# Kernel tuning notes

Measured on AMD Instinct MI355X. Metric: run time of the kernel, lower is better.

The kernel has to match this reference:

```python
import jax, jax.numpy as jnp
import numpy as np

T, L, N, DR = 8, 8, 500, 32
D = 2 * DR          # dr2 = 64
K = 12              # neighbors per region
S = 2               # number_sp attention layers


def setup_inputs() -> dict:
    key = jax.random.key(0)
    ks = jax.random.split(key, 14)
    inp = {}
    inp["all_data_static"] = jax.random.normal(ks[0], (T, L, N, D), jnp.float32)
    inp["thre_nc"] = jax.random.uniform(ks[1], (T, L, N, 1), jnp.float32)
    inp["all_data_dynamic_now"] = jax.random.uniform(ks[2], (L, N, D), jnp.float32)
    inp["neigh_poi"] = jax.random.randint(ks[3], (N, K), 0, N)
    inp["neigh_road"] = jax.random.randint(ks[4], (N, K), 0, N)
    inp["neigh_record"] = jax.random.randint(ks[5], (N, K), 0, N)
    inp["w1"] = jax.random.normal(ks[6], (2 * D, D), jnp.float32) * 0.05
    inp["wq_all"] = jax.random.normal(ks[7], (2, 3, S, D, D), jnp.float32) * 0.05
    inp["wk_all"] = jax.random.normal(ks[8], (2, 3, S, D, D), jnp.float32) * 0.05
    inp["wd_all"] = jax.random.normal(ks[9], (2, 3, S, D, D), jnp.float32) * 0.05
    inp["wmix_all"] = jax.random.normal(ks[10], (2, 3, D), jnp.float32) * 0.1
    inp["conv_w"] = jax.random.normal(ks[11], (4, 2 * D + 1), jnp.float32) * 0.05
    inp["conv_b"] = jnp.zeros((4,), jnp.float32)
    inp["fin_w"] = jax.random.normal(ks[12], (N, N), jnp.float32) * 0.02
    inp["fin_b"] = jnp.ones((N,), jnp.float32)
    return inp


def _attention(data, neigh, wq, wk, wd):
    # data: (T,L,N,D), neigh: (N,K)
    dn = data[:, :, neigh, :]                                   # (T,L,N,K,D) gather
    q = jnp.einsum('tlnd,de->tlne', data, wq)                   # (T,L,N,D)
    k = jnp.einsum('tlnkd,de->tlnke', dn, wk)                   # (T,L,N,K,D)
    a = jax.nn.softmax(jnp.einsum('tlne,tlnke->tlnk', q, k), -1)
    out = q + jnp.einsum('tlnk,tlnke->tlne', a, k)              # residual on q
    return jax.nn.sigmoid(jnp.einsum('tlnd,de->tlne', out, wd))


def _multiattention(data, neighs, wq, wk, wd, wmix):
    outs = []
    for g in range(3):  # poi, road, record
        x = data
        for s in range(wq.shape[1]):
            x = _attention(x, neighs[g], wq[g, s], wk[g, s], wd[g, s])
        outs.append(x)
    return jax.nn.sigmoid(outs[0] * wmix[0] + outs[1] * wmix[1] + outs[2] * wmix[2])


def reference(all_data_static, thre_nc, all_data_dynamic_now,
              neigh_poi, neigh_road, neigh_record,
              w1, wq_all, wk_all, wd_all, wmix_all,
              conv_w, conv_b, fin_w, fin_b):
    # --- Evolution: gated recurrence over time steps 1..T-1 ---
    def evo_step(now, xs):
        st, th = xs  # (L,N,D), (L,N,1)
        new = jax.nn.sigmoid(jnp.concatenate([now, st], -1) @ w1 * th
                             + now * (1.0 - th))
        return new, (new, new - now)
    now_final, (dyn_rest, diffs) = jax.lax.scan(
        evo_step, all_data_dynamic_now, (all_data_static[1:], thre_nc[1:]))
    all_dyn = jnp.concatenate([all_data_dynamic_now[None], dyn_rest], 0)  # (T,L,N,D)

    neighs = (neigh_poi, neigh_road, neigh_record)
    dyn = _multiattention(all_dyn, neighs, wq_all[0], wk_all[0], wd_all[0], wmix_all[0])
    sta = _multiattention(all_data_static, neighs, wq_all[1], wk_all[1], wd_all[1], wmix_all[1])
    x = jnp.concatenate([dyn, sta], -1)                          # (T,L,N,2D)

    # --- ConvLSTM, kernel (1,1), hidden_dim=1 -> pointwise gated recurrence ---
    h0 = jnp.zeros((x.shape[0], x.shape[2], 1), x.dtype)         # (T,N,1)
    def cell(carry, xt):  # xt: (T,N,2D)
        h, c = carry
        gates = jnp.concatenate([xt, h], -1) @ conv_w.T + conv_b  # (T,N,4)
        i = jax.nn.sigmoid(gates[..., 0:1])
        f = jax.nn.sigmoid(gates[..., 1:2])
        o = jax.nn.sigmoid(gates[..., 2:3])
        g = jnp.tanh(gates[..., 3:4])
        c2 = f * c + i * g
        h2 = o * jnp.tanh(c2)
        return (h2, c2), None
    (h_last, _), _ = jax.lax.scan(cell, (h0, h0), jnp.swapaxes(x, 0, 1))

    out = jax.nn.sigmoid(h_last[..., 0] @ fin_w.T + fin_b)       # (T,N)
    return out, now_final, diffs
```

## Files before the change

kernel.cpp:

```cpp
#include <hip/hip_runtime.h>
#include <math.h>

namespace {
constexpr int kT = 8, kL = 8, kN = 500, kD = 64, kK = 12;
constexpr int kLN  = kL * kN;
constexpr int kTLN = kT * kL * kN;
constexpr int kBUF = kTLN * kD;
constexpr int XS = 68;
constexpr int EVR = 16;
}

__device__ __forceinline__ float sigf(float v) { return 1.f / (1.f + __expf(-v)); }

__device__ __forceinline__ float tanh_fast(float v) {
    float e = __expf(-2.f * fabsf(v));
    float t = (1.f - e) / (1.f + e);
    return copysignf(t, v);
}

__device__ __forceinline__ float row_allreduce16(float v) {
    v += __int_as_float(__builtin_amdgcn_update_dpp(
            0, __float_as_int(v), 0xB1, 0xf, 0xf, true));
    v += __int_as_float(__builtin_amdgcn_update_dpp(
            0, __float_as_int(v), 0x4E, 0xf, 0xf, true));
    v += __int_as_float(__builtin_amdgcn_update_dpp(
            0, __float_as_int(v), 0x124, 0xf, 0xf, true));
    v += __int_as_float(__builtin_amdgcn_update_dpp(
            0, __float_as_int(v), 0x128, 0xf, 0xf, true));
    return v;
}

__device__ __forceinline__ void stage_x(const float* __restrict__ src, float* lds,
                                        int row0) {
    int r  = threadIdx.x >> 4;
    int c4 = (threadIdx.x & 15) << 2;
#pragma unroll
    for (int i = 0; i < 4; ++i) {
        int rr  = r + 16 * i;
        float4 v = *reinterpret_cast<const float4*>(src + (size_t)(row0 + rr) * 64 + c4);
        *reinterpret_cast<float4*>(lds + rr * XS + c4) = v;
    }
}

template <int K>
__device__ __forceinline__ void stage_w(const float* __restrict__ w, float* lds) {
    const float4* s = reinterpret_cast<const float4*>(w);
    float4* d = reinterpret_cast<float4*>(lds);
#pragma unroll
    for (int i = 0; i < K / 16; ++i)
        d[threadIdx.x + 256 * i] = s[threadIdx.x + 256 * i];
}

__device__ __forceinline__ void gemm_core_gw(const float* ldsx,
                                             const float* __restrict__ gw,
                                             int rblk, int cblk, float4 acc[4]) {
#pragma unroll 4
    for (int k = 0; k < 64; k += 4) {
        float4 xv[4], wv[4];
#pragma unroll
        for (int i = 0; i < 4; ++i)
            xv[i] = *reinterpret_cast<const float4*>(ldsx + (4 * rblk + i) * XS + k);
#pragma unroll
        for (int d = 0; d < 4; ++d)
            wv[d] = *reinterpret_cast<const float4*>(gw + (k + d) * 64 + 4 * cblk);
#pragma unroll
        for (int i = 0; i < 4; ++i) {
            float xs[4] = {xv[i].x, xv[i].y, xv[i].z, xv[i].w};
#pragma unroll
            for (int d = 0; d < 4; ++d) {
                acc[i].x = fmaf(xs[d], wv[d].x, acc[i].x);
                acc[i].y = fmaf(xs[d], wv[d].y, acc[i].y);
                acc[i].z = fmaf(xs[d], wv[d].z, acc[i].z);
                acc[i].w = fmaf(xs[d], wv[d].w, acc[i].w);
            }
        }
    }
}

__device__ __forceinline__ void gemm_core2_bal(const float* ldsx, const float* ldswa,
                                               const float* __restrict__ gwb,
                                               int rblk, int cblk,
                                               float4 acca[4], float4 accb[4]) {
#pragma unroll 4
    for (int k = 0; k < 64; k += 4) {
        float4 xv[4], wa[4], wb[4];
#pragma unroll
        for (int i = 0; i < 4; ++i)
            xv[i] = *reinterpret_cast<const float4*>(ldsx + (4 * rblk + i) * XS + k);
#pragma unroll
        for (int d = 0; d < 4; ++d) {
            wa[d] = *reinterpret_cast<const float4*>(ldswa + (k + d) * 64 + 4 * cblk);
            wb[d] = *reinterpret_cast<const float4*>(gwb + (k + d) * 64 + 4 * cblk);
        }
#pragma unroll
        for (int i = 0; i < 4; ++i) {
            float xs[4] = {xv[i].x, xv[i].y, xv[i].z, xv[i].w};
#pragma unroll
            for (int d = 0; d < 4; ++d) {
                acca[i].x = fmaf(xs[d], wa[d].x, acca[i].x);
                acca[i].y = fmaf(xs[d], wa[d].y, acca[i].y);
                acca[i].z = fmaf(xs[d], wa[d].z, acca[i].z);
                acca[i].w = fmaf(xs[d], wa[d].w, acca[i].w);
                accb[i].x = fmaf(xs[d], wb[d].x, accb[i].x);
                accb[i].y = fmaf(xs[d], wb[d].y, accb[i].y);
                accb[i].z = fmaf(xs[d], wb[d].z, accb[i].z);
                accb[i].w = fmaf(xs[d], wb[d].w, accb[i].w);
            }
        }
    }
}

__device__ __forceinline__ void gemm_qk_body(const float* __restrict__ X,
                                             const float* __restrict__ wq,
                                             const float* __restrict__ wk,
                                             float* __restrict__ b1c,
                                             float* __restrict__ b2c,
                                             int row0, float* ldsx, float* ldswq) {
    stage_x(X, ldsx, row0);
    stage_w<64>(wq, ldswq);
    __syncthreads();
    int rblk = threadIdx.x >> 4, cblk = threadIdx.x & 15;
    float4 aq[4] = {}, ak[4] = {};
    gemm_core2_bal(ldsx, ldswq, wk, rblk, cblk, aq, ak);
#pragma unroll
    for (int i = 0; i < 4; ++i) {
        size_t row = row0 + 4 * rblk + i;
        *reinterpret_cast<float4*>(b1c + row * 64 + 4 * cblk) = aq[i];
        *reinterpret_cast<float4*>(b2c + row * 64 + 4 * cblk) = ak[i];
    }
}

__global__ void __launch_bounds__(256) evo_statqk_kernel(
        const float* __restrict__ stat, const float* __restrict__ thre,
        const float* __restrict__ dyn0, float* __restrict__ all_dyn,
        float* __restrict__ diff, float* __restrict__ now_final,
        const float* __restrict__ w1, const float* __restrict__ wq_all,
        const float* __restrict__ wk_all, float* __restrict__ b1,
        float* __restrict__ b2) {
    __shared__ float lds[2 * EVR * XS + 128 * 64];
    if (blockIdx.x < kLN / EVR) {
        float* ldsn = lds;
        float* ldss = lds + EVR * XS;
        float* ldsw = lds + 2 * EVR * XS;
        int row0 = blockIdx.x * EVR;
        int r  = threadIdx.x >> 4;
        int c4 = (threadIdx.x & 15) << 2;
        *reinterpret_cast<float4*>(ldsn + r * XS + c4) =
            *reinterpret_cast<const float4*>(dyn0 + (size_t)(row0 + r) * 64 + c4);
        stage_w<128>(w1, ldsw);
        __syncthreads();
        {
            float4 x0 = *reinterpret_cast<const float4*>(ldsn + r * XS + c4);
            *reinterpret_cast<float4*>(all_dyn + (size_t)(row0 + r) * 64 + c4) = x0;
        }
#pragma unroll 1
        for (int t = 1; t < kT; ++t) {
            *reinterpret_cast<float4*>(ldss + r * XS + c4) =
                *reinterpret_cast<const float4*>(stat + (size_t)t * kLN * kD
                                                 + (size_t)(row0 + r) * 64 + c4);
            __syncthreads();
            float4 acc = {0.f, 0.f, 0.f, 0.f};
#pragma unroll 4
            for (int k = 0; k < 64; k += 4) {
                float4 xv = *reinterpret_cast<const float4*>(ldsn + r * XS + k);
                float xs[4] = {xv.x, xv.y, xv.z, xv.w};
#pragma unroll
                for (int d = 0; d < 4; ++d) {
                    float4 wv = *reinterpret_cast<const float4*>(ldsw + (k + d) * 64 + c4);
                    acc.x = fmaf(xs[d], wv.x, acc.x);
                    acc.y = fmaf(xs[d], wv.y, acc.y);
                    acc.z = fmaf(xs[d], wv.z, acc.z);
                    acc.w = fmaf(xs[d], wv.w, acc.w);
                }
            }
#pragma unroll 4
            for (int k = 0; k < 64; k += 4) {
                float4 xv = *reinterpret_cast<const float4*>(ldss + r * XS + k);
                float xs[4] = {xv.x, xv.y, xv.z, xv.w};
#pragma unroll
                for (int d = 0; d < 4; ++d) {
                    float4 wv = *reinterpret_cast<const float4*>(ldsw + (64 + k + d) * 64 + c4);
                    acc.x = fmaf(xs[d], wv.x, acc.x);
                    acc.y = fmaf(xs[d], wv.y, acc.y);
                    acc.z = fmaf(xs[d], wv.z, acc.z);
                    acc.w = fmaf(xs[d], wv.w, acc.w);
                }
            }
            int row = row0 + r;
            float tt = thre[t * kLN + row];
            float4 xn = *reinterpret_cast<const float4*>(ldsn + r * XS + c4);
            float4 nv;
            nv.x = sigf(acc.x * tt + xn.x * (1.f - tt));
            nv.y = sigf(acc.y * tt + xn.y * (1.f - tt));
            nv.z = sigf(acc.z * tt + xn.z * (1.f - tt));
            nv.w = sigf(acc.w * tt + xn.w * (1.f - tt));
            float4 df;
            df.x = nv.x - xn.x; df.y = nv.y - xn.y;
            df.z = nv.z - xn.z; df.w = nv.w - xn.w;
            *reinterpret_cast<float4*>(all_dyn + ((size_t)t * kLN + row) * 64 + c4) = nv;
            *reinterpret_cast<float4*>(diff + ((size_t)(t - 1) * kLN + row) * 64 + c4) = df;
            if (t == kT - 1)
                *reinterpret_cast<float4*>(now_final + (size_t)row * 64 + c4) = nv;
            __syncthreads();
            *reinterpret_cast<float4*>(ldsn + r * XS + c4) = nv;
        }
    } else {
        int b = blockIdx.x - kLN / EVR;
        int c = 3 + b / 500;
        int tile = b - (c - 3) * 500;
        float* b1c = b1 + (size_t)c * kBUF;
        float* b2c = b2 + (size_t)c * kBUF;
        size_t woff = (size_t)(c * 2) * kD * kD;
        gemm_qk_body(stat, wq_all + woff, wk_all + woff, b1c, b2c,
                     tile * 64, lds, lds + 64 * XS);
    }
}

__global__ void __launch_bounds__(256) gemm_qk(const float* __restrict__ Xdyn,
                                               const float* __restrict__ Xstat,
                                               const float* __restrict__ wq_all,
                                               const float* __restrict__ wk_all,
                                               float* __restrict__ b1,
                                               float* __restrict__ b2, int step) {
    __shared__ float ldsx[64 * XS];
    __shared__ float ldswq[64 * 64];
    int c = blockIdx.y;
    int m = c / 3;
    float* b1c = b1 + (size_t)c * kBUF;
    float* b2c = b2 + (size_t)c * kBUF;
    const float* X = step ? b1c : (m == 0 ? Xdyn : Xstat);
    size_t woff = (size_t)(c * 2 + step) * kD * kD;
    gemm_qk_body(X, wq_all + woff, wk_all + woff, b1c, b2c,
                 blockIdx.x * 64, ldsx, ldswq);
}

__global__ void __launch_bounds__(256) scorewd_kernel(float* __restrict__ b1,
                                                      const float* __restrict__ b2,
                                                      const int* __restrict__ npoi,
                                                      const int* __restrict__ nroad,
                                                      const int* __restrict__ nrec,
                                                      const float* __restrict__ wd_all,
                                                      int step) {
    __shared__ float ldsx[64 * XS];
    int p   = blockIdx.y * gridDim.x + blockIdx.x;
    int xcd = p & 7;
    int gid = xcd * 375 + (p >> 3);
    int c    = gid / 500;
    int tile = gid - c * 500;
    int g = c % 3;
    float* b1c = b1 + (size_t)c * kBUF;
    const float* b2c = b2 + (size_t)c * kBUF;
    const int* neigh = (g == 0) ? npoi : (g == 1) ? nroad : nrec;
    const float* gw = wd_all + (size_t)(c * 2 + step) * kD * kD;

    int lane = threadIdx.x & 63;
    int wv   = threadIdx.x >> 6;
    int sub  = lane >> 4;
    int gq   = lane & 15;
    int row0 = tile * 64;
#pragma unroll 1
    for (int pp = 0; pp < 4; ++pp) {
        int lr  = pp * 16 + wv * 4 + sub;
        int row = row0 + lr;
        int n   = row % kN;
        int slab = row - n;
        float4 q = *(reinterpret_cast<const float4*>(b1c) + (size_t)row * 16 + gq);
        const int4* nbp = reinterpret_cast<const int4*>(neigh + n * kK);
        int4 nb0 = nbp[0], nb1 = nbp[1], nb2 = nbp[2];
        int nb[12] = {nb0.x, nb0.y, nb0.z, nb0.w, nb1.x, nb1.y, nb1.z, nb1.w,
                      nb2.x, nb2.y, nb2.z, nb2.w};
        float4 kv[12];
        float sc[12];
#pragma unroll
        for (int j = 0; j < 12; ++j) {
            kv[j] = *(reinterpret_cast<const float4*>(b2c) + (size_t)(slab + nb[j]) * 16 + gq);
            sc[j] = q.x * kv[j].x + q.y * kv[j].y + q.z * kv[j].z + q.w * kv[j].w;
        }
#pragma unroll
        for (int j = 0; j < 12; ++j) sc[j] = row_allreduce16(sc[j]);
        float mx = sc[0];
#pragma unroll
        for (int j = 1; j < 12; ++j) mx = fmaxf(mx, sc[j]);
        float ssum = 0.f;
#pragma unroll
        for (int j = 0; j < 12; ++j) { sc[j] = __expf(sc[j] - mx); ssum += sc[j]; }
        float inv = 1.f / ssum;
        float4 o = q;
#pragma unroll
        for (int j = 0; j < 12; ++j) {
            float a = sc[j] * inv;
            o.x = fmaf(a, kv[j].x, o.x);
            o.y = fmaf(a, kv[j].y, o.y);
            o.z = fmaf(a, kv[j].z, o.z);
            o.w = fmaf(a, kv[j].w, o.w);
        }
        *reinterpret_cast<float4*>(ldsx + lr * XS + 4 * gq) = o;
    }
    __syncthreads();
    int rblk = threadIdx.x >> 4, cblk = threadIdx.x & 15;
    float4 acc[4] = {};
    gemm_core_gw(ldsx, gw, rblk, cblk, acc);
#pragma unroll
    for (int i = 0; i < 4; ++i) {
        size_t idx = ((size_t)(row0 + 4 * rblk + i)) * 64 + 4 * cblk;
        float4 y;
        y.x = sigf(acc[i].x); y.y = sigf(acc[i].y);
        y.z = sigf(acc[i].z); y.w = sigf(acc[i].w);
        *reinterpret_cast<float4*>(b1c + idx) = y;
    }
}

__global__ void __launch_bounds__(256) lstm_kernel(const float* __restrict__ b1,
                                                   const float* __restrict__ wmix,
                                                   const float* __restrict__ cw,
                                                   const float* __restrict__ cb,
                                                   float* __restrict__ hlast) {
    int lane = threadIdx.x & 63;
    int wv   = threadIdx.x >> 6;
    int sub  = lane >> 4;
    int fq   = lane & 15;
    int cell = blockIdx.x * 16 + wv * 4 + sub;
    int t = cell / kN, n = cell % kN;
    float wd_[4][4], ws_[4][4], wh[4], bb[4];
#pragma unroll
    for (int gg = 0; gg < 4; ++gg) {
#pragma unroll
        for (int k = 0; k < 4; ++k) {
            wd_[gg][k] = cw[gg * 129 + fq * 4 + k];
            ws_[gg][k] = cw[gg * 129 + 64 + fq * 4 + k];
        }
        wh[gg] = cw[gg * 129 + 128];
        bb[gg] = cb[gg];
    }
    float4 wm[6];
#pragma unroll
    for (int j = 0; j < 6; ++j)
        wm[j] = *reinterpret_cast<const float4*>(wmix + j * 64 + fq * 4);
    float h = 0.f, cc = 0.f;
#pragma unroll 1
    for (int l = 0; l < kL; ++l) {
        size_t row16 = ((size_t)(t * kL + l) * kN + n) * 16 + fq;
        float4 y[6];
#pragma unroll
        for (int j = 0; j < 6; ++j)
            y[j] = *(reinterpret_cast<const float4*>(b1) + (size_t)j * (kBUF / 4) + row16);
        float4 xd, xs;
        xd.x = sigf(y[0].x * wm[0].x + y[1].x * wm[1].x + y[2].x * wm[2].x);
        xd.y = sigf(y[0].y * wm[0].y + y[1].y * wm[1].y + y[2].y * wm[2].y);
        xd.z = sigf(y[0].z * wm[0].z + y[1].z * wm[1].z + y[2].z * wm[2].z);
        xd.w = sigf(y[0].w * wm[0].w + y[1].w * wm[1].w + y[2].w * wm[2].w);
        xs.x = sigf(y[3].x * wm[3].x + y[4].x * wm[4].x + y[5].x * wm[5].x);
        xs.y = sigf(y[3].y * wm[3].y + y[4].y * wm[4].y + y[5].y * wm[5].y);
        xs.z = sigf(y[3].z * wm[3].z + y[4].z * wm[4].z + y[5].z * wm[5].z);
        xs.w = sigf(y[3].w * wm[3].w + y[4].w * wm[4].w + y[5].w * wm[5].w);
        float gsum[4];
#pragma unroll
        for (int gg = 0; gg < 4; ++gg) {
            float v = xd.x * wd_[gg][0] + xd.y * wd_[gg][1]
                    + xd.z * wd_[gg][2] + xd.w * wd_[gg][3];
            v += xs.x * ws_[gg][0] + xs.y * ws_[gg][1]
               + xs.z * ws_[gg][2] + xs.w * ws_[gg][3];
            gsum[gg] = v;
        }
#pragma unroll
        for (int gg = 0; gg < 4; ++gg) gsum[gg] = row_allreduce16(gsum[gg]);
        float gi = sigf(gsum[0] + bb[0] + h * wh[0]);
        float gf = sigf(gsum[1] + bb[1] + h * wh[1]);
        float go = sigf(gsum[2] + bb[2] + h * wh[2]);
        float gg_ = tanh_fast(gsum[3] + bb[3] + h * wh[3]);
        cc = gf * cc + gi * gg_;
        h = go * tanh_fast(cc);
    }
    if (fq == 0) hlast[cell] = h;
}

__global__ void final_kernel(const float* __restrict__ h, const float* __restrict__ fw,
                             const float* __restrict__ fb, float* __restrict__ out) {
    int wave = threadIdx.x >> 6, lane = threadIdx.x & 63;
    int o = blockIdx.x * 4 + wave;
    int t = o / kN, m = o % kN;
    float acc = 0.f;
    for (int n = lane; n < kN; n += 64)
        acc = fmaf(h[t * kN + n], fw[(size_t)m * kN + n], acc);
#pragma unroll
    for (int off = 32; off > 0; off >>= 1) acc += __shfl_xor(acc, off);
    if (lane == 0) out[o] = sigf(acc + fb[m]);
}

extern "C" void kernel_launch(void* const* d_in, const int* in_sizes, int n_in,
                              void* d_out, int out_size, void* d_ws, size_t ws_size,
                              hipStream_t stream) {
    const float* stat   = (const float*)d_in[0];
    const float* thre   = (const float*)d_in[1];
    const float* dyn0   = (const float*)d_in[2];
    const int*   npoi   = (const int*)d_in[3];
    const int*   nroad  = (const int*)d_in[4];
    const int*   nrec   = (const int*)d_in[5];
    const float* w1     = (const float*)d_in[6];
    const float* wq_all = (const float*)d_in[7];
    const float* wk_all = (const float*)d_in[8];
    const float* wd_all = (const float*)d_in[9];
    const float* wmix   = (const float*)d_in[10];
    const float* conv_w = (const float*)d_in[11];
    const float* conv_b = (const float*)d_in[12];
    const float* fin_w  = (const float*)d_in[13];
    const float* fin_b  = (const float*)d_in[14];

    float* out       = (float*)d_out;
    float* now_final = out + kT * kN;
    float* diffs     = now_final + (size_t)kLN * kD;

    float* ws      = (float*)d_ws;
    float* all_dyn = ws;
    float* b1      = ws + (size_t)kBUF;
    float* b2      = ws + 7 * (size_t)kBUF;
    float* hlast   = ws + 13 * (size_t)kBUF;

    evo_statqk_kernel<<<kLN / EVR + 1500, 256, 0, stream>>>(
        stat, thre, dyn0, all_dyn, diffs, now_final, w1, wq_all, wk_all, b1, b2);

    dim3 dgrid(500, 3);
    dim3 agrid(500, 6);
    gemm_qk<<<dgrid, 256, 0, stream>>>(all_dyn, stat, wq_all, wk_all, b1, b2, 0);
    scorewd_kernel<<<agrid, 256, 0, stream>>>(b1, b2, npoi, nroad, nrec, wd_all, 0);
    gemm_qk<<<agrid, 256, 0, stream>>>(all_dyn, stat, wq_all, wk_all, b1, b2, 1);
    scorewd_kernel<<<agrid, 256, 0, stream>>>(b1, b2, npoi, nroad, nrec, wd_all, 1);

    lstm_kernel<<<kT * kN / 16, 256, 0, stream>>>(b1, wmix, conv_w, conv_b, hlast);
    final_kernel<<<kT * kN / 4, 256, 0, stream>>>(hlast, fin_w, fin_b, out);
}
```

Before: 304.8 us.

## Interleave dynamic and static attention stages in merged QK/score kernels

Restructures the four-launch attention schedule so each launch pairs a QK GEMM stage of one branch (dynamic or static) with a score+Wd stage of the other branch. Even blocks run QK, odd blocks run score/Wd, giving three mixed launches plus a final score kernel for the dynamic branch. The aim is to overlap compute-heavy GEMM tiles with gather-heavy scoring tiles and balance work per launch. It drops the XCD-aware block remapping the old score kernel used, and the larger LDS footprint in the mixed kernel may reduce occupancy.

```diff
diff --git a/kernel.cpp b/kernel.cpp
--- a/kernel.cpp
+++ b/kernel.cpp
@@ -127,6 +127,67 @@
         size_t row = row0 + 4 * rblk + i;
         *reinterpret_cast<float4*>(b1c + row * 64 + 4 * cblk) = aq[i];
         *reinterpret_cast<float4*>(b2c + row * 64 + 4 * cblk) = ak[i];
+    }
+}
+
+__device__ __forceinline__ void scorewd_body(float* __restrict__ b1c,
+                                             const float* __restrict__ b2c,
+                                             const int* __restrict__ neigh,
+                                             const float* __restrict__ gw,
+                                             int row0, float* ldsx) {
+    int lane = threadIdx.x & 63;
+    int wv   = threadIdx.x >> 6;
+    int sub  = lane >> 4;
+    int gq   = lane & 15;
+#pragma unroll 1
+    for (int pp = 0; pp < 4; ++pp) {
+        int lr  = pp * 16 + wv * 4 + sub;
+        int row = row0 + lr;
+        int n   = row % kN;
+        int slab = row - n;
+        float4 q = *(reinterpret_cast<const float4*>(b1c) + (size_t)row * 16 + gq);
+        const int4* nbp = reinterpret_cast<const int4*>(neigh + n * kK);
+        int4 nb0 = nbp[0], nb1 = nbp[1], nb2 = nbp[2];
+        int nb[12] = {nb0.x, nb0.y, nb0.z, nb0.w, nb1.x, nb1.y, nb1.z, nb1.w,
+                      nb2.x, nb2.y, nb2.z, nb2.w};
+        float4 kv[12];
+        float sc[12];
+#pragma unroll
+        for (int j = 0; j < 12; ++j) {
+            kv[j] = *(reinterpret_cast<const float4*>(b2c) + (size_t)(slab + nb[j]) * 16 + gq);
+            sc[j] = q.x * kv[j].x + q.y * kv[j].y + q.z * kv[j].z + q.w * kv[j].w;
+        }
+#pragma unroll
+        for (int j = 0; j < 12; ++j) sc[j] = row_allreduce16(sc[j]);
+        float mx = sc[0];
+#pragma unroll
+        for (int j = 1; j < 12; ++j) mx = fmaxf(mx, sc[j]);
+        float ssum = 0.f;
+#pragma unroll
+        for (int j = 0; j < 12; ++j) { sc[j] = __expf(sc[j] - mx); ssum += sc[j]; }
+        float inv = 1.f / ssum;
+        float4 o = q;
+#pragma unroll
+        for (int j = 0; j < 12; ++j) {
+            float a = sc[j] * inv;
+            o.x = fmaf(a, kv[j].x, o.x);
+            o.y = fmaf(a, kv[j].y, o.y);
+            o.z = fmaf(a, kv[j].z, o.z);
+            o.w = fmaf(a, kv[j].w, o.w);
+        }
+        *reinterpret_cast<float4*>(ldsx + lr * XS + 4 * gq) = o;
+    }
+    __syncthreads();
+    int rblk = threadIdx.x >> 4, cblk = threadIdx.x & 15;
+    float4 acc[4] = {};
+    gemm_core_gw(ldsx, gw, rblk, cblk, acc);
+#pragma unroll
+    for (int i = 0; i < 4; ++i) {
+        size_t idx = ((size_t)(row0 + 4 * rblk + i)) * 64 + 4 * cblk;
+        float4 y;
+        y.x = sigf(acc[i].x); y.y = sigf(acc[i].y);
+        y.z = sigf(acc[i].z); y.w = sigf(acc[i].w);
+        *reinterpret_cast<float4*>(b1c + idx) = y;
     }
 }
 
@@ -216,98 +277,52 @@
     }
 }
 
-__global__ void __launch_bounds__(256) gemm_qk(const float* __restrict__ Xdyn,
-                                               const float* __restrict__ Xstat,
-                                               const float* __restrict__ wq_all,
-                                               const float* __restrict__ wk_all,
-                                               float* __restrict__ b1,
-                                               float* __restrict__ b2, int step) {
+__global__ void __launch_bounds__(256) qk_sw_kernel(
+        float* __restrict__ b1, float* __restrict__ b2,
+        const float* __restrict__ Xdyn, const float* __restrict__ Xstat,
+        const float* __restrict__ wq_all, const float* __restrict__ wk_all,
+        const float* __restrict__ wd_all, const int* __restrict__ npoi,
+        const int* __restrict__ nroad, const int* __restrict__ nrec,
+        int qk_cbase, int qk_step, int sw_cbase, int sw_step) {
+    __shared__ float lds[64 * XS + 64 * 64];
+    int b = blockIdx.x;
+    int idx = b >> 1;
+    int cof = idx / 500;
+    int tile = idx - cof * 500;
+    if ((b & 1) == 0) {
+        int c = qk_cbase + cof;
+        float* b1c = b1 + (size_t)c * kBUF;
+        float* b2c = b2 + (size_t)c * kBUF;
+        const float* X = qk_step ? b1c : (c < 3 ? Xdyn : Xstat);
+        size_t woff = (size_t)(c * 2 + qk_step) * kD * kD;
+        gemm_qk_body(X, wq_all + woff, wk_all + woff, b1c, b2c,
+                     tile * 64, lds, lds + 64 * XS);
+    } else {
+        int c = sw_cbase + cof;
+        int g = c % 3;
+        const int* neigh = (g == 0) ? npoi : (g == 1) ? nroad : nrec;
+        float* b1c = b1 + (size_t)c * kBUF;
+        const float* b2c = b2 + (size_t)c * kBUF;
+        const float* gw = wd_all + (size_t)(c * 2 + sw_step) * kD * kD;
+        scorewd_body(b1c, b2c, neigh, gw, tile * 64, lds);
+    }
+}
+
+__global__ void __launch_bounds__(256) scorewd3_kernel(float* __restrict__ b1,
+                                                       const float* __restrict__ b2,
+                                                       const int* __restrict__ npoi,
+                                                       const int* __restrict__ nroad,
+                                                       const int* __restrict__ nrec,
+                                                       const float* __restrict__ wd_all,
+                                                       int cbase, int step) {
     __shared__ float ldsx[64 * XS];
-    __shared__ float ldswq[64 * 64];
-    int c = blockIdx.y;
-    int m = c / 3;
-    float* b1c = b1 + (size_t)c * kBUF;
-    float* b2c = b2 + (size_t)c * kBUF;
-    const float* X = step ? b1c : (m == 0 ? Xdyn : Xstat);
-    size_t woff = (size_t)(c * 2 + step) * kD * kD;
-    gemm_qk_body(X, wq_all + woff, wk_all + woff, b1c, b2c,
-                 blockIdx.x * 64, ldsx, ldswq);
-}
-
-__global__ void __launch_bounds__(256) scorewd_kernel(float* __restrict__ b1,
-                                                      const float* __restrict__ b2,
-                                                      const int* __restrict__ npoi,
-                                                      const int* __restrict__ nroad,
-                                                      const int* __restrict__ nrec,
-                                                      const float* __restrict__ wd_all,
-                                                      int step) {
-    __shared__ float ldsx[64 * XS];
-    int p   = blockIdx.y * gridDim.x + blockIdx.x;
-    int xcd = p & 7;
-    int gid = xcd * 375 + (p >> 3);
-    int c    = gid / 500;
-    int tile = gid - c * 500;
+    int c = cbase + blockIdx.y;
     int g = c % 3;
+    const int* neigh = (g == 0) ? npoi : (g == 1) ? nroad : nrec;
     float* b1c = b1 + (size_t)c * kBUF;
     const float* b2c = b2 + (size_t)c * kBUF;
-    const int* neigh = (g == 0) ? npoi : (g == 1) ? nroad : nrec;
     const float* gw = wd_all + (size_t)(c * 2 + step) * kD * kD;
-
-    int lane = threadIdx.x & 63;
-    int wv   = threadIdx.x >> 6;
-    int sub  = lane >> 4;
-    int gq   = lane & 15;
-    int row0 = tile * 64;
-#pragma unroll 1
-    for (int pp = 0; pp < 4; ++pp) {
-        int lr  = pp * 16 + wv * 4 + sub;
-        int row = row0 + lr;
-        int n   = row % kN;
-        int slab = row - n;
-        float4 q = *(reinterpret_cast<const float4*>(b1c) + (size_t)row * 16 + gq);
-        const int4* nbp = reinterpret_cast<const int4*>(neigh + n * kK);
-        int4 nb0 = nbp[0], nb1 = nbp[1], nb2 = nbp[2];
-        int nb[12] = {nb0.x, nb0.y, nb0.z, nb0.w, nb1.x, nb1.y, nb1.z, nb1.w,
-                      nb2.x, nb2.y, nb2.z, nb2.w};
-        float4 kv[12];
-        float sc[12];
-#pragma unroll
-        for (int j = 0; j < 12; ++j) {
-            kv[j] = *(reinterpret_cast<const float4*>(b2c) + (size_t)(slab + nb[j]) * 16 + gq);
-            sc[j] = q.x * kv[j].x + q.y * kv[j].y + q.z * kv[j].z + q.w * kv[j].w;
-        }
-#pragma unroll
-        for (int j = 0; j < 12; ++j) sc[j] = row_allreduce16(sc[j]);
-        float mx = sc[0];
-#pragma unroll
-        for (int j = 1; j < 12; ++j) mx = fmaxf(mx, sc[j]);
-        float ssum = 0.f;
-#pragma unroll
-        for (int j = 0; j < 12; ++j) { sc[j] = __expf(sc[j] - mx); ssum += sc[j]; }
-        float inv = 1.f / ssum;
-        float4 o = q;
-#pragma unroll
-        for (int j = 0; j < 12; ++j) {
-            float a = sc[j] * inv;
-            o.x = fmaf(a, kv[j].x, o.x);
-            o.y = fmaf(a, kv[j].y, o.y);
-            o.z = fmaf(a, kv[j].z, o.z);
-            o.w = fmaf(a, kv[j].w, o.w);
-        }
-        *reinterpret_cast<float4*>(ldsx + lr * XS + 4 * gq) = o;
-    }
-    __syncthreads();
-    int rblk = threadIdx.x >> 4, cblk = threadIdx.x & 15;
-    float4 acc[4] = {};
-    gemm_core_gw(ldsx, gw, rblk, cblk, acc);
-#pragma unroll
-    for (int i = 0; i < 4; ++i) {
-        size_t idx = ((size_t)(row0 + 4 * rblk + i)) * 64 + 4 * cblk;
-        float4 y;
-        y.x = sigf(acc[i].x); y.y = sigf(acc[i].y);
-        y.z = sigf(acc[i].z); y.w = sigf(acc[i].w);
-        *reinterpret_cast<float4*>(b1c + idx) = y;
-    }
+    scorewd_body(b1c, b2c, neigh, gw, blockIdx.x * 64, ldsx);
 }
 
 __global__ void __launch_bounds__(256) lstm_kernel(const float* __restrict__ b1,
@@ -418,13 +433,15 @@
 
     evo_statqk_kernel<<<kLN / EVR + 1500, 256, 0, stream>>>(
         stat, thre, dyn0, all_dyn, diffs, now_final, w1, wq_all, wk_all, b1, b2);
-
-    dim3 dgrid(500, 3);
-    dim3 agrid(500, 6);
-    gemm_qk<<<dgrid, 256, 0, stream>>>(all_dyn, stat, wq_all, wk_all, b1, b2, 0);
-    scorewd_kernel<<<agrid, 256, 0, stream>>>(b1, b2, npoi, nroad, nrec, wd_all, 0);
-    gemm_qk<<<agrid, 256, 0, stream>>>(all_dyn, stat, wq_all, wk_all, b1, b2, 1);
-    scorewd_kernel<<<agrid, 256, 0, stream>>>(b1, b2, npoi, nroad, nrec, wd_all, 1);
+    qk_sw_kernel<<<3000, 256, 0, stream>>>(b1, b2, all_dyn, stat, wq_all, wk_all,
+                                           wd_all, npoi, nroad, nrec, 0, 0, 3, 0);
+    qk_sw_kernel<<<3000, 256, 0, stream>>>(b1, b2, all_dyn, stat, wq_all, wk_all,
+                                           wd_all, npoi, nroad, nrec, 3, 1, 0, 0);
+    qk_sw_kernel<<<3000, 256, 0, stream>>>(b1, b2, all_dyn, stat, wq_all, wk_all,
+                                           wd_all, npoi, nroad, nrec, 0, 1, 3, 1);
+    dim3 sgrid3(500, 3);
+    scorewd3_kernel<<<sgrid3, 256, 0, stream>>>(b1, b2, npoi, nroad, nrec,
+                                                wd_all, 0, 1);
 
     lstm_kernel<<<kT * kN / 16, 256, 0, stream>>>(b1, wmix, conv_w, conv_b, hlast);
     final_kernel<<<kT * kN / 4, 256, 0, stream>>>(hlast, fin_w, fin_b, out);
```

Result: slower. 371.0 us (+21.7%).
